# Kernel tuning notes

Measured on AMD Instinct MI355X. Metric: run time of the kernel, lower is better.

The kernel has to match this reference:

```python
import jax, jax.numpy as jnp
import numpy as np

D_MODEL = 2048
N_HEAD = 16
N_KV_HEAD = 4
D_HEAD = D_MODEL // N_HEAD          # 128
N_REP = N_HEAD // N_KV_HEAD        # 4
B, S = 2, 2048


def setup_inputs() -> dict:
    key = jax.random.key(0)
    ks = jax.random.split(key, 7)
    x = jax.random.normal(ks[0], (B, S, D_MODEL), dtype=jnp.float32)
    cos = jax.random.uniform(ks[1], (S, D_HEAD // 2), dtype=jnp.float32)
    sin = jax.random.uniform(ks[2], (S, D_HEAD // 2), dtype=jnp.float32)
    sc = 1.0 / np.sqrt(D_MODEL)
    # weights stored as [in, out] so projection is x @ W
    wq = jax.random.normal(ks[3], (D_MODEL, D_MODEL), dtype=jnp.float32) * sc
    wk = jax.random.normal(ks[4], (D_MODEL, N_KV_HEAD * D_HEAD), dtype=jnp.float32) * sc
    wv = jax.random.normal(ks[5], (D_MODEL, N_KV_HEAD * D_HEAD), dtype=jnp.float32) * sc
    wo = jax.random.normal(ks[6], (D_MODEL, D_MODEL), dtype=jnp.float32) * sc
    return {"x": x, "cos": cos, "sin": sin, "wq": wq, "wk": wk, "wv": wv, "wo": wo}


def _apply_rope(t, cos, sin):
    # t: [B, H, S, D_HEAD]; cos/sin: [S, D_HEAD//2]
    d = t.shape[-1] // 2
    t1, t2 = t[..., :d], t[..., d:]
    c = cos[None, None, :, :]
    s = sin[None, None, :, :]
    return jnp.concatenate([t1 * c - t2 * s, t2 * c + t1 * s], axis=-1)


def reference(x, cos, sin, wq, wk, wv, wo):
    b, s, _ = x.shape
    q = (x @ wq).reshape(b, s, N_HEAD, D_HEAD).transpose(0, 2, 1, 3)      # [B,H,S,d]
    k = (x @ wk).reshape(b, s, N_KV_HEAD, D_HEAD).transpose(0, 2, 1, 3)   # [B,Hk,S,d]
    v = (x @ wv).reshape(b, s, N_KV_HEAD, D_HEAD).transpose(0, 2, 1, 3)
    q = _apply_rope(q, cos, sin)
    k = _apply_rope(k, cos, sin)
    # group query heads by shared kv head (repeat_interleave => consecutive groups)
    qg = q.reshape(b, N_KV_HEAD, N_REP, s, D_HEAD)
    scale = 1.0 / jnp.sqrt(jnp.asarray(D_HEAD, dtype=q.dtype))
    scores = jnp.einsum('bkrsd,bktd->bkrst', qg, k) * scale               # [B,Hk,r,S,S]
    causal = jnp.tril(jnp.ones((s, s), dtype=bool))
    scores = jnp.where(causal, scores, jnp.asarray(-jnp.inf, dtype=scores.dtype))
    attn = jax.nn.softmax(scores, axis=-1)
    out = jnp.einsum('bkrst,bktd->bkrsd', attn, v)                        # [B,Hk,r,S,d]
    out = out.reshape(b, N_HEAD, s, D_HEAD).transpose(0, 2, 1, 3).reshape(b, s, D_MODEL)
    return out @ wo
```

## Files before the change

kernel.cpp:

```cpp
#include <hip/hip_runtime.h>
#include <stdint.h>

#define D_MODEL 2048
#define NHEAD 16
#define NKV 4
#define DHEAD 128
#define BB 2
#define SS 2048
#define MROWS (BB*SS)
#define NQKV 3072

typedef __bf16 bf16x8_t __attribute__((ext_vector_type(8)));
typedef float f32x4_t __attribute__((ext_vector_type(4)));
typedef float f32x16_t __attribute__((ext_vector_type(16)));
typedef unsigned short u16x8_t __attribute__((ext_vector_type(8)));
typedef unsigned short u16x4_t __attribute__((ext_vector_type(4)));
typedef unsigned int u32x4_t __attribute__((ext_vector_type(4)));

__device__ __forceinline__ unsigned short f2bf(float f) {
    return __builtin_bit_cast(unsigned short, (__bf16)f);
}
__device__ __forceinline__ float bf2f(unsigned short h) {
    union { uint32_t u; float f; } v; v.u = ((uint32_t)h) << 16;
    return v.f;
}
__device__ __forceinline__ unsigned int pack_bf2(float lo, float hi) {
    return (unsigned int)f2bf(lo) | ((unsigned int)f2bf(hi) << 16);
}

__device__ __forceinline__ void stage16(const unsigned short* g, unsigned short* l) {
    auto gp = (const __attribute__((address_space(1))) unsigned short*)(uintptr_t)g;
    auto lp = (__attribute__((address_space(3))) unsigned short*)(uint32_t)(uintptr_t)l;
    __builtin_amdgcn_global_load_lds(gp, lp, 16, 0, 0);
}
__device__ __forceinline__ bf16x8_t lds_frag(const unsigned short* p) {
    return __builtin_bit_cast(bf16x8_t, *(const u16x8_t*)p);
}

#define BAR()   do { __builtin_amdgcn_s_barrier(); asm volatile("" ::: "memory"); } while (0)
#define WAITL() asm volatile("s_waitcnt lgkmcnt(0)" ::: "memory")

__global__ void k_convert(const float* __restrict__ in, unsigned short* __restrict__ out, int n4) {
    int stride = gridDim.x * blockDim.x;
    for (int idx = blockIdx.x * blockDim.x + threadIdx.x; idx < n4; idx += stride) {
        float4 f = ((const float4*)in)[idx];
        u16x4_t o;
        o[0] = f2bf(f.x); o[1] = f2bf(f.y); o[2] = f2bf(f.z); o[3] = f2bf(f.w);
        ((u16x4_t*)out)[idx] = o;
    }
}

__global__ __launch_bounds__(256) void k_transpose_all(const float* __restrict__ wq,
                                                       const float* __restrict__ wk,
                                                       const float* __restrict__ wv,
                                                       const float* __restrict__ wo,
                                                       unsigned short* __restrict__ wqkvT,
                                                       unsigned short* __restrict__ woT) {
    int id = blockIdx.x;
    const float* in; unsigned short* out; int R, C, cx, ry;
    if (id < 1024)      { in = wq; out = wqkvT;                              R = 2048; C = 2048; cx = id & 31; ry = id >> 5; }
    else if (id < 1280) { id -= 1024; in = wk; out = wqkvT + (size_t)2048 * 2048; R = 2048; C = 512; cx = id & 7; ry = id >> 3; }
    else if (id < 1536) { id -= 1280; in = wv; out = wqkvT + (size_t)2560 * 2048; R = 2048; C = 512; cx = id & 7; ry = id >> 3; }
    else                { id -= 1536; in = wo; out = woT;                    R = 2048; C = 2048; cx = id & 31; ry = id >> 5; }
    const int c0 = cx * 64, r0 = ry * 64;
    __shared__ unsigned short tile[64][72];
    const int t = threadIdx.x;
    #pragma unroll
    for (int i = 0; i < 4; i++) {
        int g = i * 256 + t;
        int r = g >> 4, c4 = (g & 15) * 4;
        float4 f = *(const float4*)&in[(size_t)(r0 + r) * C + c0 + c4];
        tile[r][c4 + 0] = f2bf(f.x); tile[r][c4 + 1] = f2bf(f.y);
        tile[r][c4 + 2] = f2bf(f.z); tile[r][c4 + 3] = f2bf(f.w);
    }
    __syncthreads();
    #pragma unroll
    for (int i = 0; i < 2; i++) {
        int g = i * 256 + t;
        int oc = g >> 3, r8 = (g & 7) * 8;
        u16x8_t o;
        #pragma unroll
        for (int k = 0; k < 8; k++) o[k] = tile[r8 + k][oc];
        *(u16x8_t*)&out[(size_t)(c0 + oc) * R + r0 + r8] = o;
    }
}

__global__ void k_rope(const unsigned short* __restrict__ in, const float* __restrict__ cosb,
                       const float* __restrict__ sinb, unsigned short* __restrict__ out,
                       int nheads, int in_row_stride, float scale) {
    int idx = blockIdx.x * blockDim.x + threadIdx.x;
    int total = BB * SS * nheads * 64;
    if (idx >= total) return;
    int d  = idx & 63;
    int hh = (idx >> 6) % nheads;
    int bs = (idx >> 6) / nheads;
    int s  = bs % SS, b = bs / SS;
    const unsigned short* ip = in + (size_t)(b * SS + s) * in_row_stride + hh * 128 + d;
    float t1 = bf2f(ip[0]), t2 = bf2f(ip[64]);
    float c = cosb[s * 64 + d], sn = sinb[s * 64 + d];
    unsigned short* op = out + ((size_t)(b * nheads + hh) * SS + s) * 128 + d;
    op[0]  = f2bf((t1 * c - t2 * sn) * scale);
    op[64] = f2bf((t2 * c + t1 * sn) * scale);
}

__global__ __launch_bounds__(256) void k_vtrans(const unsigned short* __restrict__ src,
                                                unsigned short* __restrict__ vt,
                                                int stride, int colbase) {
    const int s0 = blockIdx.x * 64;
    const int kvb = blockIdx.y;
    const int b = kvb >> 2, kv = kvb & 3;
    __shared__ unsigned short tile[64][136];
    const int t = threadIdx.x;
    #pragma unroll
    for (int i = 0; i < 4; i++) {
        int g = i * 256 + t;
        int sr = g >> 4, c8 = (g & 15) * 8;
        u16x8_t v = *(const u16x8_t*)&src[(size_t)(b * SS + s0 + sr) * stride + colbase + kv * 128 + c8];
        #pragma unroll
        for (int k = 0; k < 8; k++) tile[sr][c8 + k] = v[k];
    }
    __syncthreads();
    unsigned short* obase = vt + (size_t)kvb * DHEAD * SS;
    #pragma unroll
    for (int i = 0; i < 4; i++) {
        int g = i * 256 + t;
        int d = g >> 3, s8 = (g & 7) * 8;
        u16x8_t o;
        #pragma unroll
        for (int k = 0; k < 8; k++) o[k] = tile[s8 + k][d];
        *(u16x8_t*)&obase[(size_t)d * SS + s0 + s8] = o;
    }
}

template <bool OUTF32>
__global__ __launch_bounds__(512, 2) void k_gemm8(const unsigned short* __restrict__ A,
                                                  const unsigned short* __restrict__ Bt,
                                                  void* __restrict__ Cout,
                                                  int N, int K, int ntn) {
    __shared__ __align__(16) unsigned short As[2][256 * 64];
    __shared__ __align__(16) unsigned short Bs[2][256 * 64];
    const int nwg = gridDim.x, wg = blockIdx.x;
    const int qq = nwg >> 3, rr = nwg & 7;
    const int xcd = wg & 7, sid = wg >> 3;
    const int swg = (xcd < rr ? xcd * (qq + 1) : rr * (qq + 1) + (xcd - rr) * qq) + sid;
    const int m0 = (swg / ntn) * 256, n0 = (swg % ntn) * 256;

    const int tid = threadIdx.x, lane = tid & 63, wid = tid >> 6;
    const int lr = lane & 15, lg = lane >> 4;
    const int wr = (wid >> 2) * 128, wc = (wid & 3) * 64;
    const int NT = K >> 6;

    auto stage = [&](int tile, int pos) {
        int srcTile = tile < NT ? tile : NT - 1;
        bool isA = (pos == 0) || (pos == 3);
        int half = (pos >= 2) ? 1 : 0;
        const unsigned short* base = isA ? A : Bt;
        int row0 = (isA ? m0 : n0) + half * 128;
        unsigned short* lbase = (isA ? As[tile & 1] : Bs[tile & 1]) + half * 8192;
        int k0 = srcTile * 64;
        #pragma unroll
        for (int i = 0; i < 2; i++) {
            int g = i * 512 + tid;
            int row = g >> 3, p = g & 7;
            stage16(&base[(size_t)(row0 + row) * K + k0 + ((p ^ (row & 7)) * 8)],
                    &lbase[(i * 512 + wid * 64) * 8]);
        }
    };

    bf16x8_t aA[4][2], bLo[2][2], bHi[2][2];
    f32x4_t acc[8][4] = {};

    stage(0, 0); stage(0, 3); stage(0, 1); stage(0, 2);
    stage(1, 1); stage(1, 2);
    asm volatile("s_waitcnt vmcnt(4)" ::: "memory");
    BAR();

    for (int t = 0; t < NT; t++) {
        const unsigned short* as = As[t & 1];
        const unsigned short* bs = Bs[t & 1];
        #pragma unroll
        for (int i = 0; i < 4; i++)
          #pragma unroll
          for (int kk = 0; kk < 2; kk++) {
            int R = wr + i * 16 + lr;
            aA[i][kk] = lds_frag(&as[R * 64 + (((kk * 4 + lg) ^ (R & 7)) * 8)]);
          }
        #pragma unroll
        for (int j = 0; j < 2; j++)
          #pragma unroll
          for (int kk = 0; kk < 2; kk++) {
            int R = wc + j * 16 + lr;
            bLo[j][kk] = lds_frag(&bs[R * 64 + (((kk * 4 + lg) ^ (R & 7)) * 8)]);
          }
        stage(t + 1, 0);
        BAR(); WAITL();
        __builtin_amdgcn_s_setprio(1);
        #pragma unroll
        for (int kk = 0; kk < 2; kk++)
          #pragma unroll
          for (int i = 0; i < 4; i++)
            #pragma unroll
            for (int j = 0; j < 2; j++)
              acc[i][j] = __builtin_amdgcn_mfma_f32_16x16x32_bf16(aA[i][kk], bLo[j][kk], acc[i][j], 0, 0, 0);
        __builtin_amdgcn_s_setprio(0);
        BAR();
        #pragma unroll
        for (int j = 0; j < 2; j++)
          #pragma unroll
          for (int kk = 0; kk < 2; kk++) {
            int R = wc + (2 + j) * 16 + lr;
            bHi[j][kk] = lds_frag(&bs[R * 64 + (((kk * 4 + lg) ^ (R & 7)) * 8)]);
          }
        stage(t + 1, 3);
        BAR(); WAITL();
        __builtin_amdgcn_s_setprio(1);
        #pragma unroll
        for (int kk = 0; kk < 2; kk++)
          #pragma unroll
          for (int i = 0; i < 4; i++)
            #pragma unroll
            for (int j = 0; j < 2; j++)
              acc[i][2 + j] = __builtin_amdgcn_mfma_f32_16x16x32_bf16(aA[i][kk], bHi[j][kk], acc[i][2 + j], 0, 0, 0);
        __builtin_amdgcn_s_setprio(0);
        BAR();
        #pragma unroll
        for (int i = 0; i < 4; i++)
          #pragma unroll
          for (int kk = 0; kk < 2; kk++) {
            int R = wr + (4 + i) * 16 + lr;
            aA[i][kk] = lds_frag(&as[R * 64 + (((kk * 4 + lg) ^ (R & 7)) * 8)]);
          }
        stage(t + 2, 1);
        BAR(); WAITL();
        __builtin_amdgcn_s_setprio(1);
        #pragma unroll
        for (int kk = 0; kk < 2; kk++)
          #pragma unroll
          for (int i = 0; i < 4; i++)
            #pragma unroll
            for (int j = 0; j < 2; j++)
              acc[4 + i][2 + j] = __builtin_amdgcn_mfma_f32_16x16x32_bf16(aA[i][kk], bHi[j][kk], acc[4 + i][2 + j], 0, 0, 0);
        __builtin_amdgcn_s_setprio(0);
        BAR();
        stage(t + 2, 2);
        asm volatile("s_waitcnt vmcnt(4)" ::: "memory");
        BAR(); WAITL();
        __builtin_amdgcn_s_setprio(1);
        #pragma unroll
        for (int kk = 0; kk < 2; kk++)
          #pragma unroll
          for (int i = 0; i < 4; i++)
            #pragma unroll
            for (int j = 0; j < 2; j++)
              acc[4 + i][j] = __builtin_amdgcn_mfma_f32_16x16x32_bf16(aA[i][kk], bLo[j][kk], acc[4 + i][j], 0, 0, 0);
        __builtin_amdgcn_s_setprio(0);
        BAR();
    }

    #pragma unroll
    for (int m = 0; m < 8; m++)
      #pragma unroll
      for (int n = 0; n < 4; n++)
        #pragma unroll
        for (int r = 0; r < 4; r++) {
            int row = m0 + wr + m * 16 + lg * 4 + r;
            int col = n0 + wc + n * 16 + lr;
            if constexpr (OUTF32) ((float*)Cout)[(size_t)row * N + col] = acc[m][n][r];
            else ((unsigned short*)Cout)[(size_t)row * N + col] = f2bf(acc[m][n][r]);
        }
}

template <bool OUTF32>
__global__ __launch_bounds__(512, 2) void k_gemm8h(const unsigned short* __restrict__ A,
                                                   const unsigned short* __restrict__ Bt,
                                                   void* __restrict__ Cout,
                                                   int N, int K, int ntn) {
    __shared__ __align__(16) unsigned short As[2][128 * 64];
    __shared__ __align__(16) unsigned short Bs[2][256 * 64];
    const int nwg = gridDim.x, wg = blockIdx.x;
    const int qq = nwg >> 3, rr = nwg & 7;
    const int xcd = wg & 7, sid = wg >> 3;
    const int swg = (xcd < rr ? xcd * (qq + 1) : rr * (qq + 1) + (xcd - rr) * qq) + sid;
    const int m0 = (swg / ntn) * 128, n0 = (swg % ntn) * 256;

    const int tid = threadIdx.x, lane = tid & 63, wid = tid >> 6;
    const int lr = lane & 15, lg = lane >> 4;
    const int wr = (wid >> 2) * 64, wc = (wid & 3) * 64;
    const int NT = K >> 6;

    auto stage = [&](int tile, int pos) {
        int srcTile = tile < NT ? tile : NT - 1;
        bool isA = (pos == 0);
        const unsigned short* base = isA ? A : Bt;
        int row0 = isA ? m0 : (n0 + (pos - 1) * 128);
        unsigned short* lbase = isA ? As[tile & 1] : (Bs[tile & 1] + (pos - 1) * 8192);
        int k0 = srcTile * 64;
        #pragma unroll
        for (int i = 0; i < 2; i++) {
            int g = i * 512 + tid;
            int row = g >> 3, p = g & 7;
            stage16(&base[(size_t)(row0 + row) * K + k0 + ((p ^ (row & 7)) * 8)],
                    &lbase[(i * 512 + wid * 64) * 8]);
        }
    };

    bf16x8_t aA[2][2], bLo[2][2], bHi[2][2];
    f32x4_t acc[4][4] = {};

    stage(0, 0); stage(0, 1); stage(0, 2);
    stage(1, 1); stage(1, 2);
    asm volatile("s_waitcnt vmcnt(4)" ::: "memory");
    BAR();

    for (int t = 0; t < NT; t++) {
        const unsigned short* as = As[t & 1];
        const unsigned short* bs = Bs[t & 1];
        #pragma unroll
        for (int i = 0; i < 2; i++)
          #pragma unroll
          for (int kk = 0; kk < 2; kk++) {
            int R = wr + i * 16 + lr;
            aA[i][kk] = lds_frag(&as[R * 64 + (((kk * 4 + lg) ^ (R & 7)) * 8)]);
          }
        #pragma unroll
        for (int j = 0; j < 2; j++)
          #pragma unroll
          for (int kk = 0; kk < 2; kk++) {
            int R = wc + j * 16 + lr;
            bLo[j][kk] = lds_frag(&bs[R * 64 + (((kk * 4 + lg) ^ (R & 7)) * 8)]);
          }
        stage(t + 1, 0);
        BAR(); WAITL();
        __builtin_amdgcn_s_setprio(1);
        #pragma unroll
        for (int kk = 0; kk < 2; kk++)
          #pragma unroll
          for (int i = 0; i < 2; i++)
            #pragma unroll
            for (int j = 0; j < 2; j++)
              acc[i][j] = __builtin_amdgcn_mfma_f32_16x16x32_bf16(aA[i][kk], bLo[j][kk], acc[i][j], 0, 0, 0);
        __builtin_amdgcn_s_setprio(0);
        BAR();
        #pragma unroll
        for (int j = 0; j < 2; j++)
          #pragma unroll
          for (int kk = 0; kk < 2; kk++) {
            int R = wc + (2 + j) * 16 + lr;
            bHi[j][kk] = lds_frag(&bs[R * 64 + (((kk * 4 + lg) ^ (R & 7)) * 8)]);
          }
        BAR(); WAITL();
        __builtin_amdgcn_s_setprio(1);
        #pragma unroll
        for (int kk = 0; kk < 2; kk++)
          #pragma unroll
          for (int i = 0; i < 2; i++)
            #pragma unroll
            for (int j = 0; j < 2; j++)
              acc[i][2 + j] = __builtin_amdgcn_mfma_f32_16x16x32_bf16(aA[i][kk], bHi[j][kk], acc[i][2 + j], 0, 0, 0);
        __builtin_amdgcn_s_setprio(0);
        BAR();
        #pragma unroll
        for (int i = 0; i < 2; i++)
          #pragma unroll
          for (int kk = 0; kk < 2; kk++) {
            int R = wr + (2 + i) * 16 + lr;
            aA[i][kk] = lds_frag(&as[R * 64 + (((kk * 4 + lg) ^ (R & 7)) * 8)]);
          }
        stage(t + 2, 1);
        BAR(); WAITL();
        __builtin_amdgcn_s_setprio(1);
        #pragma unroll
        for (int kk = 0; kk < 2; kk++)
          #pragma unroll
          for (int i = 0; i < 2; i++)
            #pragma unroll
            for (int j = 0; j < 2; j++)
              acc[2 + i][2 + j] = __builtin_amdgcn_mfma_f32_16x16x32_bf16(aA[i][kk], bHi[j][kk], acc[2 + i][2 + j], 0, 0, 0);
        __builtin_amdgcn_s_setprio(0);
        BAR();
        stage(t + 2, 2);
        asm volatile("s_waitcnt vmcnt(4)" ::: "memory");
        BAR(); WAITL();
        __builtin_amdgcn_s_setprio(1);
        #pragma unroll
        for (int kk = 0; kk < 2; kk++)
          #pragma unroll
          for (int i = 0; i < 2; i++)
            #pragma unroll
            for (int j = 0; j < 2; j++)
              acc[2 + i][j] = __builtin_amdgcn_mfma_f32_16x16x32_bf16(aA[i][kk], bLo[j][kk], acc[2 + i][j], 0, 0, 0);
        __builtin_amdgcn_s_setprio(0);
        BAR();
    }

    #pragma unroll
    for (int m = 0; m < 4; m++)
      #pragma unroll
      for (int n = 0; n < 4; n++)
        #pragma unroll
        for (int r = 0; r < 4; r++) {
            int row = m0 + wr + m * 16 + lg * 4 + r;
            int col = n0 + wc + n * 16 + lr;
            if constexpr (OUTF32) ((float*)Cout)[(size_t)row * N + col] = acc[m][n][r];
            else ((unsigned short*)Cout)[(size_t)row * N + col] = f2bf(acc[m][n][r]);
        }
}

__global__ __launch_bounds__(256, 2) void k_attn(const unsigned short* __restrict__ qg,
                                                 const float* __restrict__ cosb,
                                                 const float* __restrict__ sinb,
                                                 const unsigned short* __restrict__ kb,
                                                 const unsigned short* __restrict__ vt,
                                                 unsigned short* __restrict__ ab) {
    const int bid = blockIdx.x;
    const int xcd = bid & 7, sid = bid >> 3;
    const int b = xcd >> 2, kvh = xcd & 3;
    int t, hh;
    if (sid < 32) { t = sid >> 1; hh = sid & 1; }
    else { int s2 = sid - 32; t = 15 - (s2 >> 1); hh = 2 + (s2 & 1); }
    const int h = kvh * 4 + hh;
    const int tid = threadIdx.x, lane = tid & 63, wid = tid >> 6;
    const int ql = lane & 31, hi = lane >> 5;
    const int swzq = ql & 7;
    __shared__ __align__(16) unsigned short k_lds[2][64 * 128];
    __shared__ __align__(16) unsigned short v_lds[2][128 * 64];
    __shared__ float sm_lds[128];

    const unsigned short* kbase = kb + (size_t)(b * NKV + kvh) * SS * DHEAD;
    const unsigned short* vbase = vt + (size_t)(b * NKV + kvh) * DHEAD * SS;

    auto stage_kv = [&](int j, int buf) {
        #pragma unroll
        for (int i = 0; i < 4; i++) {
            int g = i * 256 + wid * 64 + lane;
            int row = g >> 4, p = g & 15;
            stage16(&kbase[(size_t)(j * 64 + row) * DHEAD + ((p ^ (row & 7)) * 8)],
                    &k_lds[buf][(i * 256 + wid * 64) * 8]);
        }
        #pragma unroll
        for (int i = 0; i < 4; i++) {
            int g = i * 256 + wid * 64 + lane;
            int row = g >> 3, p = g & 7;
            stage16(&vbase[(size_t)row * SS + j * 64 + ((p ^ (row & 7)) * 8)],
                    &v_lds[buf][(i * 256 + wid * 64) * 8]);
        }
    };

    auto make_frag = [&](const f32x16_t& p, int base) -> bf16x8_t {
        unsigned int c01 = pack_bf2(p[base + 0], p[base + 1]);
        unsigned int c23 = pack_bf2(p[base + 2], p[base + 3]);
        unsigned int c45 = pack_bf2(p[base + 4], p[base + 5]);
        unsigned int c67 = pack_bf2(p[base + 6], p[base + 7]);
        unsigned int r1 = __shfl_xor(hi ? c01 : c45, 32);
        unsigned int r2 = __shfl_xor(hi ? c23 : c67, 32);
        u32x4_t w;
        w[0] = hi ? r1 : c01;
        w[1] = hi ? r2 : c23;
        w[2] = hi ? c45 : r1;
        w[3] = hi ? c67 : r2;
        return __builtin_bit_cast(bf16x8_t, w);
    };

    const int q0w = t * 128 + wid * 32;
    const int s_row = q0w + ql;
    const int jend = 2 * t + 1;

    bf16x8_t qf[8];
    {
        const unsigned short* qsrc = qg + (size_t)(b * SS + s_row) * NQKV + h * DHEAD;
        const float SCALE = 0.12751743f;
        #pragma unroll
        for (int kk = 0; kk < 4; kk++) {
            int dbase = kk * 16 + hi * 8;
            u16x8_t r1 = *(const u16x8_t*)&qsrc[dbase];
            u16x8_t r2 = *(const u16x8_t*)&qsrc[64 + dbase];
            float4 c0 = *(const float4*)&cosb[(size_t)s_row * 64 + dbase];
            float4 c1 = *(const float4*)&cosb[(size_t)s_row * 64 + dbase + 4];
            float4 s0 = *(const float4*)&sinb[(size_t)s_row * 64 + dbase];
            float4 s1 = *(const float4*)&sinb[(size_t)s_row * 64 + dbase + 4];
            float cc[8] = {c0.x, c0.y, c0.z, c0.w, c1.x, c1.y, c1.z, c1.w};
            float ss[8] = {s0.x, s0.y, s0.z, s0.w, s1.x, s1.y, s1.z, s1.w};
            #pragma unroll
            for (int e = 0; e < 8; e++) {
                float t1 = bf2f(r1[e]), t2 = bf2f(r2[e]);
                qf[kk][e]     = (__bf16)((t1 * cc[e] - t2 * ss[e]) * SCALE);
                qf[kk + 4][e] = (__bf16)((t2 * cc[e] + t1 * ss[e]) * SCALE);
            }
        }
    }

    f32x16_t acc[4] = {};
    float m_i = -1e30f, l_i = 0.f;

    stage_kv(0, 0);
    asm volatile("s_waitcnt vmcnt(0)" ::: "memory");
    __syncthreads();

    #pragma unroll 1
    for (int j = 0; j <= jend; j++) {
        const int buf = j & 1;
        if (j < jend) stage_kv(j + 1, buf ^ 1);
        if ((q0w + 31) >= (j << 6)) {
            const unsigned short* kl = k_lds[buf];
            const unsigned short* vl = v_lds[buf];
            f32x16_t p0 = {}, p1 = {};
            __builtin_amdgcn_s_setprio(1);
            #pragma unroll
            for (int kk = 0; kk < 8; kk++) {
                int c = ((2 * kk + hi) ^ swzq) * 8;
                bf16x8_t k0 = lds_frag(&kl[ql * 128 + c]);
                bf16x8_t k1 = lds_frag(&kl[(32 + ql) * 128 + c]);
                p0 = __builtin_amdgcn_mfma_f32_32x32x16_bf16(k0, qf[kk], p0, 0, 0, 0);
                p1 = __builtin_amdgcn_mfma_f32_32x32x16_bf16(k1, qf[kk], p1, 0, 0, 0);
            }
            __builtin_amdgcn_s_setprio(0);
            if ((j << 6) + 63 > q0w) {
                const int qg2 = q0w + ql;
                const int kvb = (j << 6) + 4 * hi;
                #pragma unroll
                for (int r = 0; r < 16; r++) {
                    int kvg = kvb + (r & 3) + 8 * (r >> 2);
                    if (kvg > qg2) p0[r] = -1e30f;
                    if (kvg + 32 > qg2) p1[r] = -1e30f;
                }
            }
            float mx = p0[0];
            #pragma unroll
            for (int r = 1; r < 16; r++) mx = fmaxf(mx, p0[r]);
            #pragma unroll
            for (int r = 0; r < 16; r++) mx = fmaxf(mx, p1[r]);
            mx = fmaxf(mx, __shfl_xor(mx, 32));
            if (__any(mx - m_i > 8.0f)) {
                float mnew = fmaxf(m_i, mx);
                float alpha = exp2f(m_i - mnew);
                l_i *= alpha; m_i = mnew;
                if (lane < 32) sm_lds[wid * 32 + lane] = alpha;
                WAITL();
                #pragma unroll
                for (int r = 0; r < 16; r++) {
                    float ar = sm_lds[wid * 32 + (r & 3) + 8 * (r >> 2) + 4 * hi];
                    #pragma unroll
                    for (int d = 0; d < 4; d++) acc[d][r] *= ar;
                }
            }
            float sum = 0.f;
            #pragma unroll
            for (int r = 0; r < 16; r++) { float v = exp2f(p0[r] - m_i); p0[r] = v; sum += v; }
            #pragma unroll
            for (int r = 0; r < 16; r++) { float v = exp2f(p1[r] - m_i); p1[r] = v; sum += v; }
            sum += __shfl_xor(sum, 32);
            l_i += sum;
            bf16x8_t pa[4];
            pa[0] = make_frag(p0, 0);
            pa[1] = make_frag(p0, 8);
            pa[2] = make_frag(p1, 0);
            pa[3] = make_frag(p1, 8);
            __builtin_amdgcn_s_setprio(1);
            #pragma unroll
            for (int ks = 0; ks < 4; ks++) {
                int cv = ((2 * ks + hi) ^ swzq) * 8;
                #pragma unroll
                for (int d = 0; d < 4; d++) {
                    bf16x8_t bv = lds_frag(&vl[(d * 32 + ql) * 64 + cv]);
                    acc[d] = __builtin_amdgcn_mfma_f32_32x32x16_bf16(pa[ks], bv, acc[d], 0, 0, 0);
                }
            }
            __builtin_amdgcn_s_setprio(0);
        }
        asm volatile("s_waitcnt vmcnt(0)" ::: "memory");
        __syncthreads();
    }

    if (lane < 32) sm_lds[wid * 32 + lane] = l_i;
    WAITL();
    #pragma unroll
    for (int r = 0; r < 16; r++) {
        float li = sm_lds[wid * 32 + (r & 3) + 8 * (r >> 2) + 4 * hi];
        float rl = 1.0f / li;
        int rowg = q0w + (r & 3) + 8 * (r >> 2) + 4 * hi;
        #pragma unroll
        for (int d = 0; d < 4; d++)
            ab[((size_t)b * SS + rowg) * D_MODEL + h * DHEAD + d * 32 + ql] =
                f2bf(acc[d][r] * rl);
    }
}

extern "C" void kernel_launch(void* const* d_in, const int* in_sizes, int n_in,
                              void* d_out, int out_size, void* d_ws, size_t ws_size,
                              hipStream_t stream) {
    const float* x    = (const float*)d_in[0];
    const float* cosb = (const float*)d_in[1];
    const float* sinb = (const float*)d_in[2];
    const float* wq   = (const float*)d_in[3];
    const float* wk   = (const float*)d_in[4];
    const float* wv   = (const float*)d_in[5];
    const float* wo   = (const float*)d_in[6];

    char* ws = (char*)d_ws;
    unsigned short* xb    = (unsigned short*)(ws + (size_t)0);
    unsigned short* wqkvT = (unsigned short*)(ws + ((size_t)16 << 20));
    unsigned short* woT   = (unsigned short*)(ws + ((size_t)28 << 20));
    unsigned short* qkvg  = (unsigned short*)(ws + ((size_t)36 << 20));
    unsigned short* abuf  = (unsigned short*)(ws + ((size_t)60 << 20));
    unsigned short* kbuf  = (unsigned short*)(ws + ((size_t)76 << 20));
    unsigned short* vtb   = (unsigned short*)(ws + ((size_t)80 << 20));

    k_convert<<<2048, 256, 0, stream>>>(x, xb, MROWS * D_MODEL / 4);
    k_transpose_all<<<2560, 256, 0, stream>>>(wq, wk, wv, wo, wqkvT, woT);

    k_gemm8<false><<<16 * 12, 512, 0, stream>>>(xb, wqkvT, qkvg, NQKV, D_MODEL, 12);

    k_rope<<<(BB * SS * NKV * 64) / 256, 256, 0, stream>>>(qkvg + 2048, cosb, sinb, kbuf, NKV, NQKV, 1.0f);
    k_vtrans<<<dim3(32, 8), 256, 0, stream>>>(qkvg, vtb, NQKV, 2560);

    k_attn<<<512, 256, 0, stream>>>(qkvg, cosb, sinb, kbuf, vtb, abuf);

    k_gemm8h<true><<<32 * 8, 512, 0, stream>>>(abuf, woT, (float*)d_out, D_MODEL, D_MODEL, 8);
}
```

Before: 196.5 us.

## Software-pipeline QK^T of next KV tile with softmax of current tile

Splits K and V staging so K is prefetched two tiles ahead and V one tile ahead. The QK^T MFMAs for tile j+1 are issued before the softmax and PV of tile j, so matrix-core work overlaps the exp/max/sum VALU work. The loop is unrolled by two with ping-pong score registers. Max and sum reductions become tree reductions to shorten dependency chains. The extra live score accumulators raise VGPR pressure, which may reduce occupancy or cause spills.

```diff
diff --git a/kernel.cpp b/kernel.cpp
--- a/kernel.cpp
+++ b/kernel.cpp
@@ -429,20 +429,24 @@
     const unsigned short* kbase = kb + (size_t)(b * NKV + kvh) * SS * DHEAD;
     const unsigned short* vbase = vt + (size_t)(b * NKV + kvh) * DHEAD * SS;
 
-    auto stage_kv = [&](int j, int buf) {
+    auto stage_k = [&](int j) {
+        unsigned short* dst = k_lds[j & 1];
         #pragma unroll
         for (int i = 0; i < 4; i++) {
             int g = i * 256 + wid * 64 + lane;
             int row = g >> 4, p = g & 15;
             stage16(&kbase[(size_t)(j * 64 + row) * DHEAD + ((p ^ (row & 7)) * 8)],
-                    &k_lds[buf][(i * 256 + wid * 64) * 8]);
-        }
+                    &dst[(i * 256 + wid * 64) * 8]);
+        }
+    };
+    auto stage_v = [&](int j) {
+        unsigned short* dst = v_lds[j & 1];
         #pragma unroll
         for (int i = 0; i < 4; i++) {
             int g = i * 256 + wid * 64 + lane;
             int row = g >> 3, p = g & 7;
             stage16(&vbase[(size_t)row * SS + j * 64 + ((p ^ (row & 7)) * 8)],
-                    &v_lds[buf][(i * 256 + wid * 64) * 8]);
+                    &dst[(i * 256 + wid * 64) * 8]);
         }
     };
 
@@ -489,47 +493,54 @@
         }
     }
 
+    auto do_qk = [&](int jt, f32x16_t& o0, f32x16_t& o1) {
+        const unsigned short* kl = k_lds[jt & 1];
+        o0 = (f32x16_t){}; o1 = (f32x16_t){};
+        #pragma unroll
+        for (int kk = 0; kk < 8; kk++) {
+            int c = ((2 * kk + hi) ^ swzq) * 8;
+            bf16x8_t k0 = lds_frag(&kl[ql * 128 + c]);
+            bf16x8_t k1 = lds_frag(&kl[(32 + ql) * 128 + c]);
+            o0 = __builtin_amdgcn_mfma_f32_32x32x16_bf16(k0, qf[kk], o0, 0, 0, 0);
+            o1 = __builtin_amdgcn_mfma_f32_32x32x16_bf16(k1, qf[kk], o1, 0, 0, 0);
+        }
+    };
+
     f32x16_t acc[4] = {};
     float m_i = -1e30f, l_i = 0.f;
-
-    stage_kv(0, 0);
+    f32x16_t pa0, pa1, pb0, pb1;
+
+    stage_v(0); stage_k(0);
     asm volatile("s_waitcnt vmcnt(0)" ::: "memory");
     __syncthreads();
-
-    #pragma unroll 1
-    for (int j = 0; j <= jend; j++) {
+    do_qk(0, pa0, pa1);
+    stage_k(1);
+    __syncthreads();
+
+    auto iter_body = [&](int j, f32x16_t& pc0, f32x16_t& pc1, f32x16_t& pn0, f32x16_t& pn1) {
         const int buf = j & 1;
-        if (j < jend) stage_kv(j + 1, buf ^ 1);
+        if (j + 1 <= jend) stage_v(j + 1);
+        if (j + 2 <= jend) stage_k(j + 2);
         if ((q0w + 31) >= (j << 6)) {
-            const unsigned short* kl = k_lds[buf];
-            const unsigned short* vl = v_lds[buf];
-            f32x16_t p0 = {}, p1 = {};
-            __builtin_amdgcn_s_setprio(1);
-            #pragma unroll
-            for (int kk = 0; kk < 8; kk++) {
-                int c = ((2 * kk + hi) ^ swzq) * 8;
-                bf16x8_t k0 = lds_frag(&kl[ql * 128 + c]);
-                bf16x8_t k1 = lds_frag(&kl[(32 + ql) * 128 + c]);
-                p0 = __builtin_amdgcn_mfma_f32_32x32x16_bf16(k0, qf[kk], p0, 0, 0, 0);
-                p1 = __builtin_amdgcn_mfma_f32_32x32x16_bf16(k1, qf[kk], p1, 0, 0, 0);
-            }
-            __builtin_amdgcn_s_setprio(0);
             if ((j << 6) + 63 > q0w) {
                 const int qg2 = q0w + ql;
                 const int kvb = (j << 6) + 4 * hi;
                 #pragma unroll
                 for (int r = 0; r < 16; r++) {
                     int kvg = kvb + (r & 3) + 8 * (r >> 2);
-                    if (kvg > qg2) p0[r] = -1e30f;
-                    if (kvg + 32 > qg2) p1[r] = -1e30f;
+                    if (kvg > qg2) pc0[r] = -1e30f;
+                    if (kvg + 32 > qg2) pc1[r] = -1e30f;
                 }
             }
-            float mx = p0[0];
-            #pragma unroll
-            for (int r = 1; r < 16; r++) mx = fmaxf(mx, p0[r]);
-            #pragma unroll
-            for (int r = 0; r < 16; r++) mx = fmaxf(mx, p1[r]);
-            mx = fmaxf(mx, __shfl_xor(mx, 32));
+            if (j < jend && (q0w + 31) >= ((j + 1) << 6)) do_qk(j + 1, pn0, pn1);
+            f32x16_t mm;
+            #pragma unroll
+            for (int r = 0; r < 16; r++) mm[r] = fmaxf(pc0[r], pc1[r]);
+            #pragma unroll
+            for (int s = 8; s >= 1; s >>= 1)
+                #pragma unroll
+                for (int r = 0; r < 8; r++) if (r < s) mm[r] = fmaxf(mm[r], mm[r + s]);
+            float mx = fmaxf(mm[0], __shfl_xor(mm[0], 32));
             if (__any(mx - m_i > 8.0f)) {
                 float mnew = fmaxf(m_i, mx);
                 float alpha = exp2f(m_i - mnew);
@@ -543,18 +554,24 @@
                     for (int d = 0; d < 4; d++) acc[d][r] *= ar;
                 }
             }
-            float sum = 0.f;
-            #pragma unroll
-            for (int r = 0; r < 16; r++) { float v = exp2f(p0[r] - m_i); p0[r] = v; sum += v; }
-            #pragma unroll
-            for (int r = 0; r < 16; r++) { float v = exp2f(p1[r] - m_i); p1[r] = v; sum += v; }
-            sum += __shfl_xor(sum, 32);
-            l_i += sum;
-            bf16x8_t pa[4];
-            pa[0] = make_frag(p0, 0);
-            pa[1] = make_frag(p0, 8);
-            pa[2] = make_frag(p1, 0);
-            pa[3] = make_frag(p1, 8);
+            f32x16_t sv;
+            #pragma unroll
+            for (int r = 0; r < 16; r++) {
+                float v0 = exp2f(pc0[r] - m_i); pc0[r] = v0;
+                float v1 = exp2f(pc1[r] - m_i); pc1[r] = v1;
+                sv[r] = v0 + v1;
+            }
+            #pragma unroll
+            for (int s = 8; s >= 1; s >>= 1)
+                #pragma unroll
+                for (int r = 0; r < 8; r++) if (r < s) sv[r] += sv[r + s];
+            l_i += sv[0] + __shfl_xor(sv[0], 32);
+            bf16x8_t pfr[4];
+            pfr[0] = make_frag(pc0, 0);
+            pfr[1] = make_frag(pc0, 8);
+            pfr[2] = make_frag(pc1, 0);
+            pfr[3] = make_frag(pc1, 8);
+            const unsigned short* vl = v_lds[buf];
             __builtin_amdgcn_s_setprio(1);
             #pragma unroll
             for (int ks = 0; ks < 4; ks++) {
@@ -562,13 +579,19 @@
                 #pragma unroll
                 for (int d = 0; d < 4; d++) {
                     bf16x8_t bv = lds_frag(&vl[(d * 32 + ql) * 64 + cv]);
-                    acc[d] = __builtin_amdgcn_mfma_f32_32x32x16_bf16(pa[ks], bv, acc[d], 0, 0, 0);
+                    acc[d] = __builtin_amdgcn_mfma_f32_32x32x16_bf16(pfr[ks], bv, acc[d], 0, 0, 0);
                 }
             }
             __builtin_amdgcn_s_setprio(0);
         }
         asm volatile("s_waitcnt vmcnt(0)" ::: "memory");
         __syncthreads();
+    };
+
+    #pragma unroll 1
+    for (int j = 0; j <= jend; j += 2) {
+        iter_body(j, pa0, pa1, pb0, pb1);
+        iter_body(j + 1, pb0, pb1, pa0, pa1);
     }
 
     if (lane < 32) sm_lds[wid * 32 + lane] = l_i;
```

Result: slower. 201.7 us (+2.6%).
